# Performance work log

Measured on AMD Instinct MI355X. Metric: run time of the kernel, lower is better.

The kernel has to match this reference:

```python
import jax, jax.numpy as jnp
import numpy as np

FORGET_BIAS = 1.0

def _lstm_scan(x_seq, W, b, c0, h0):
    """x_seq: [T, B, D]; W: [D+H, 4H] (gate order i,j,f,o as in BasicLSTMCell)."""
    def step(carry, x_t):
        c, h = carry
        gates = jnp.dot(jnp.concatenate([x_t, h], axis=-1), W) + b  # [B, 4H]
        i, j, f, o = jnp.split(gates, 4, axis=-1)
        c_new = c * jax.nn.sigmoid(f + FORGET_BIAS) + jax.nn.sigmoid(i) * jnp.tanh(j)
        h_new = jnp.tanh(c_new) * jax.nn.sigmoid(o)
        return (c_new, h_new), h_new
    (c_T, h_T), hs = jax.lax.scan(step, (c0, h0), x_seq)
    return hs, (c_T, h_T)


def setup_inputs() -> dict:
    key = jax.random.key(0)
    ks = jax.random.split(key, 10)
    B, T_enc, D_in = 128, 64, 2048
    T_dec, D_w, H, V = 32, 300, 512, 32000
    s = lambda fan_in: 1.0 / np.sqrt(fan_in)
    return {
        "frames": jax.random.normal(ks[0], (B, T_enc, D_in), dtype=jnp.float32),
        "caption_ids": jax.random.randint(ks[1], (B, T_dec), 0, V, dtype=jnp.int32),
        "emb_table": jax.random.normal(ks[2], (V, D_w), dtype=jnp.float32) * 0.1,
        "W_enc": jax.random.normal(ks[3], (D_in + H, 4 * H), dtype=jnp.float32) * s(D_in + H),
        "b_enc": jnp.zeros((4 * H,), dtype=jnp.float32),
        "W_dec": jax.random.normal(ks[4], (D_w + H, 4 * H), dtype=jnp.float32) * s(D_w + H),
        "b_dec": jnp.zeros((4 * H,), dtype=jnp.float32),
        "W_out": jax.random.normal(ks[5], (H, D_w), dtype=jnp.float32) * s(H),
        "b_out": jnp.zeros((D_w,), dtype=jnp.float32),
    }


def reference(frames, caption_ids, emb_table, W_enc, b_enc, W_dec, b_dec, W_out, b_out):
    B, _, _ = frames.shape
    H = W_out.shape[0]
    c0 = jnp.zeros((B, H), dtype=frames.dtype)
    h0 = jnp.zeros((B, H), dtype=frames.dtype)

    # Encoder: dynamic_rnn over frames (dropout keep_prob=1 -> identity)
    _, enc_state = _lstm_scan(jnp.swapaxes(frames, 0, 1), W_enc, b_enc, c0, h0)

    # Decoder: teacher-forced over caption embeddings, starting from encoder state
    cap_emb = emb_table[caption_ids]                       # [B, T_dec, D_w]
    dec_hs, _ = _lstm_scan(jnp.swapaxes(cap_emb, 0, 1), W_dec, b_dec, *enc_state)  # [T_dec, B, H]

    # hidden_to_word dense per timestep
    word_vecs = jnp.einsum('tbh,hw->tbw', dec_hs, W_out) + b_out  # [T_dec, B, D_w]
    return jnp.swapaxes(word_vecs, 0, 1)                   # [B, T_dec, D_w]
```

## Files before the change

kernel.cpp:

```cpp
#include <hip/hip_runtime.h>
#include <stdint.h>

typedef unsigned short u16;
typedef __attribute__((ext_vector_type(4))) float f32x4;
typedef __attribute__((ext_vector_type(8))) short short8;
typedef __attribute__((ext_vector_type(4))) unsigned short u16x4;
typedef __attribute__((ext_vector_type(4))) int int4v;

__device__ __forceinline__ u16 f2b(float f) {
  uint32_t u = __float_as_uint(f);
  uint32_t r = (u + 0x7fffu + ((u >> 16) & 1u)) >> 16;
  return (u16)r;
}
__device__ __forceinline__ float b2f(u16 b) {
  return __uint_as_float(((uint32_t)b) << 16);
}
__device__ __forceinline__ float sigm(float x) { return 1.f / (1.f + __expf(-x)); }
__device__ __forceinline__ float tanh_fast(float x) {
  float e = __expf(2.f * x);
  return 1.f - 2.f / (e + 1.f);
}
__device__ __forceinline__ void gl2lds16(const void* g, void* l) {
  __builtin_amdgcn_global_load_lds((const __attribute__((address_space(1))) void*)g,
                                   (__attribute__((address_space(3))) void*)l, 16, 0, 0);
}

__global__ void cvt_bf16_kernel(const float* __restrict__ in, u16* __restrict__ out, int n4) {
  int i = blockIdx.x * 256 + threadIdx.x;
  if (i >= n4) return;
  float4 v = ((const float4*)in)[i];
  u16x4 o = { f2b(v.x), f2b(v.y), f2b(v.z), f2b(v.w) };
  *(u16x4*)(out + (size_t)i * 4) = o;
}

__global__ void transpose_kernel(const float* __restrict__ W, u16* __restrict__ WT,
                                 int ldin, int ldout, int xreal, int xpad) {
  __shared__ float tile[64][65];
  const int kb = blockIdx.x * 64;
  const int pb = blockIdx.y * 64;
  const int t = threadIdx.x;
  const int pc = t & 63;
  const int kr4 = t >> 6;
#pragma unroll
  for (int it = 0; it < 16; ++it) {
    int kl = kr4 + it * 4;
    int kc = kb + kl;
    int ko = kc < xpad ? kc : kc - (xpad - xreal);
    bool valid = (kc < xreal) || (kc >= xpad);
    tile[kl][pc] = valid ? W[(size_t)ko * ldin + pb + pc] : 0.f;
  }
  __syncthreads();
  const int pl = t >> 2;
  const int kq = t & 3;
#pragma unroll
  for (int half = 0; half < 2; ++half) {
    union { short8 v; u16 a[8]; } pk;
#pragma unroll
    for (int i = 0; i < 8; ++i) pk.a[i] = f2b(tile[kq * 16 + half * 8 + i][pl]);
    *(short8*)&WT[(size_t)(pb + pl) * ldout + kb + kq * 16 + half * 8] = pk.v;
  }
}

__global__ void woutT_kernel(const float* __restrict__ Wout, u16* __restrict__ WT) {
  int idx = blockIdx.x * 256 + threadIdx.x;
  if (idx >= 384 * 512) return;
  int n = idx >> 9, k = idx & 511;
  float v = (n < 300) ? Wout[(size_t)k * 300 + n] : 0.f;
  WT[idx] = f2b(v);
}

__global__ void embed_kernel(const int* __restrict__ ids, const float* __restrict__ emb,
                             u16* __restrict__ Adec) {
  int r = blockIdx.x;
  int t = r >> 7, b = r & 127;
  int id = ids[b * 32 + t];
  const float* src = emb + (size_t)id * 300;
  u16* dst = Adec + (size_t)r * 320;
  for (int d = threadIdx.x; d < 320; d += 64)
    dst[d] = f2b(d < 300 ? src[d] : 0.f);
}

template <int MODE>
__global__ __launch_bounds__(256)
void gemm_kernel(const u16* __restrict__ A, int lda,
                 const u16* __restrict__ BT, int ldb,
                 void* __restrict__ Cv, const float* __restrict__ bias, int K) {
  __shared__ u16 atile[128 * 32];
  __shared__ u16 btile[128 * 32];
  const int tid = threadIdx.x;
  const int wave = tid >> 6;
  const int lane = tid & 63;
  const int m0 = blockIdx.x * 128;
  const int n0 = blockIdx.y * 128;
  const int wm = wave & 1;
  const int wn = wave >> 1;
  const int colq = lane & 15;
  const int rquad = lane >> 4;

  f32x4 acc[4][4];
#pragma unroll
  for (int i = 0; i < 4; ++i)
#pragma unroll
    for (int j = 0; j < 4; ++j) { f32x4 z = {0.f, 0.f, 0.f, 0.f}; acc[i][j] = z; }

  for (int k0 = 0; k0 < K; k0 += 32) {
#pragma unroll
    for (int c = 0; c < 2; ++c) {
      const int ch = wave + c * 4;
      const int slot = ch * 64 + lane;
      const int m = slot >> 2;
      const int koff = (slot & 3) * 8;
      gl2lds16(A + (size_t)(m0 + m) * lda + k0 + koff, atile + ch * 512);
      gl2lds16(BT + (size_t)(n0 + m) * ldb + k0 + koff, btile + ch * 512);
    }
    __builtin_amdgcn_s_waitcnt(0);
    __syncthreads();
    short8 af[4], bf[4];
#pragma unroll
    for (int i = 0; i < 4; ++i)
      af[i] = *(const short8*)(atile + (wm * 64 + i * 16 + colq) * 32 + rquad * 8);
#pragma unroll
    for (int j = 0; j < 4; ++j)
      bf[j] = *(const short8*)(btile + (wn * 64 + j * 16 + colq) * 32 + rquad * 8);
#pragma unroll
    for (int i = 0; i < 4; ++i)
#pragma unroll
      for (int j = 0; j < 4; ++j)
        acc[i][j] = __builtin_amdgcn_mfma_f32_16x16x32_bf16(af[i], bf[j], acc[i][j], 0, 0, 0);
    __syncthreads();
  }

  const int gm_base = m0 + wm * 64;
  const int gn_base = n0 + wn * 64;
#pragma unroll
  for (int i = 0; i < 4; ++i) {
#pragma unroll
    for (int j = 0; j < 4; ++j) {
      const int gn = gn_base + j * 16 + colq;
      float bv;
      if (MODE == 2) bv = (gn < 300) ? bias[gn] : 0.f;
      else bv = bias[gn];
      const int rbase = gm_base + i * 16 + rquad * 4;
#pragma unroll
      for (int r = 0; r < 4; ++r) {
        const float v = acc[i][j][r] + bv;
        const int row = rbase + r;
        if (MODE == 0) {
          ((u16*)Cv)[(size_t)((row & 63) * 128 + (row >> 6)) * 2048 + gn] = f2b(v);
        } else if (MODE == 1) {
          ((u16*)Cv)[(size_t)row * 2048 + gn] = f2b(v);
        } else {
          if (gn < 300)
            ((float*)Cv)[(size_t)((row & 127) * 32 + (row >> 7)) * 300 + gn] = v;
        }
      }
    }
  }
}

__global__ __launch_bounds__(128)
void lstm_recurrent_kernel(const u16* __restrict__ pre_enc,
                           const u16* __restrict__ pre_dec,
                           const u16* __restrict__ WencT,
                           const u16* __restrict__ WdecT,
                           int* __restrict__ hbuf,
                           u16* __restrict__ dec_hs,
                           int* __restrict__ flags) {
  const int tid = threadIdx.x;
  const int lane = tid & 63;
  const int hb = tid >> 6;
  const int bg = blockIdx.x & 7;
  const int hg = blockIdx.x >> 3;
  const int colq = lane & 15;
  const int rquad = lane >> 4;

  __shared__ u16 wlds[128][520];
  __shared__ u16 stage[2][16][32];

  {
    for (int i = tid; i < 128 * 64; i += 128) {
      int lr = i >> 6, cc = i & 63;
      const u16* src = WencT + (size_t)((lr >> 5) * 512 + hg * 32 + (lr & 31)) * 2560 + 2048;
      *(short8*)&wlds[lr][cc * 8] = *(const short8*)(src + cc * 8);
    }
  }
  __syncthreads();

  float cst[4] = {0.f, 0.f, 0.f, 0.f};
  const int brow = bg * 16 + rquad * 4;
  const int pbase = hg * 32 + hb * 16 + colq;

  union HV { int4v i; short8 s; };

  for (int s = 0; s < 96; ++s) {
    const bool dec = (s >= 64);
    const u16* pre_t = dec ? (pre_dec + (size_t)(s - 64) * 262144)
                           : (pre_enc + (size_t)s * 262144);
    f32x4 acc[4];
#pragma unroll
    for (int l = 0; l < 4; ++l)
#pragma unroll
      for (int r = 0; r < 4; ++r)
        acc[l][r] = b2f(pre_t[(size_t)(brow + r) * 2048 + l * 512 + pbase]);

    if (s > 0) {
      const int* fp = flags + ((size_t)s * 8 + bg) * 16 + (lane & 15);
      while (__hip_atomic_load(fp, __ATOMIC_RELAXED, __HIP_MEMORY_SCOPE_AGENT) == 0) {}
      asm volatile("" ::: "memory");
    }

    HV hv[16];
    const int* hread = hbuf + (size_t)s * 32768 + bg * 4096 + colq * 16 + rquad * 4;
#pragma unroll
    for (int g = 0; g < 4; ++g) {
      const int* hp = hread + g * 1024;
#pragma unroll
      for (int q = 0; q < 4; ++q)
        asm volatile("global_load_dwordx4 %0, %1, off offset:%2 sc0 sc1"
                     : "=v"(hv[g * 4 + q].i) : "v"(hp), "i"(q * 1024) : "memory");
    }
    asm volatile("s_waitcnt vmcnt(0)" ::: "memory");
#pragma unroll
    for (int kt = 0; kt < 16; ++kt)
      asm volatile("" : "+v"(hv[kt].i));

#pragma unroll
    for (int kt = 0; kt < 16; ++kt) {
#pragma unroll
      for (int l = 0; l < 4; ++l) {
        short8 bf = *(const short8*)&wlds[l * 32 + hb * 16 + colq][kt * 32 + rquad * 8];
        acc[l] = __builtin_amdgcn_mfma_f32_16x16x32_bf16(hv[kt].s, bf, acc[l], 0, 0, 0);
      }
    }

    const int sb = s & 1;
#pragma unroll
    for (int r = 0; r < 4; ++r) {
      float iv = acc[0][r], jv = acc[1][r], fv = acc[2][r], ov = acc[3][r];
      float cn = cst[r] * sigm(fv + 1.f) + sigm(iv) * tanh_fast(jv);
      cst[r] = cn;
      float hvv = tanh_fast(cn) * sigm(ov);
      stage[sb][rquad * 4 + r][hb * 16 + colq] = f2b(hvv);
    }
    __syncthreads();

    if (tid < 64) {
      const int row = tid >> 2, q = tid & 3;
      union { short8 v; int4v i; } vv;
      vv.v = *(const short8*)&stage[sb][row][q * 8];
      int* dst = hbuf + (size_t)(s + 1) * 32768 + bg * 4096 + hg * 256 + row * 16 + q * 4;
      asm volatile("global_store_dwordx4 %0, %1, off sc0 sc1"
                   :: "v"(dst), "v"(vv.i) : "memory");
      if (dec)
        *(short8*)&dec_hs[(size_t)(s - 64) * 65536 + (size_t)(bg * 16 + row) * 512 +
                          hg * 32 + q * 8] = vv.v;
      asm volatile("s_waitcnt vmcnt(0)" ::: "memory");
      if (tid == 0) {
        int* fp = flags + ((size_t)(s + 1) * 8 + bg) * 16 + hg;
        int one = 1;
        asm volatile("global_store_dword %0, %1, off sc0 sc1"
                     :: "v"(fp), "v"(one) : "memory");
      }
    }

    if (s == 63) {
      for (int i = tid; i < 128 * 64; i += 128) {
        int lr = i >> 6, cc = i & 63;
        const u16* src = WdecT + (size_t)((lr >> 5) * 512 + hg * 32 + (lr & 31)) * 832 + 320;
        *(short8*)&wlds[lr][cc * 8] = *(const short8*)(src + cc * 8);
      }
      __syncthreads();
    }
  }
  asm volatile("s_waitcnt vmcnt(0)" ::: "memory");
}

extern "C" void kernel_launch(void* const* d_in, const int* in_sizes, int n_in,
                              void* d_out, int out_size, void* d_ws, size_t ws_size,
                              hipStream_t stream) {
  const float* frames = (const float*)d_in[0];
  const int* cap_ids  = (const int*)d_in[1];
  const float* emb    = (const float*)d_in[2];
  const float* W_enc  = (const float*)d_in[3];
  const float* b_enc  = (const float*)d_in[4];
  const float* W_dec  = (const float*)d_in[5];
  const float* b_dec  = (const float*)d_in[6];
  const float* W_out  = (const float*)d_in[7];
  const float* b_out  = (const float*)d_in[8];
  float* out = (float*)d_out;

  char* ws = (char*)d_ws;
  size_t off = 0;
  auto alloc = [&](size_t bytes) {
    void* p = ws + off;
    off += (bytes + 255) & ~(size_t)255;
    return p;
  };
  u16* A_enc   = (u16*)alloc(8192ull * 2048 * 2);
  u16* WencT   = (u16*)alloc(2048ull * 2560 * 2);
  u16* pre_enc = (u16*)alloc(64ull * 128 * 2048 * 2);
  u16* A_dec   = (u16*)alloc(4096ull * 320 * 2);
  u16* WdecT   = (u16*)alloc(2048ull * 832 * 2);
  u16* pre_dec = (u16*)alloc(32ull * 128 * 2048 * 2);
  u16* WoutT   = (u16*)alloc(384ull * 512 * 2);
  u16* dec_hs  = (u16*)alloc(32ull * 128 * 512 * 2);
  int* hbuf    = (int*)alloc(97ull * 32768 * 4);
  int* flags   = (int*)alloc(97ull * 8 * 16 * 4);

  hipMemsetAsync(hbuf, 0, 32768ull * 4, stream);
  hipMemsetAsync(flags, 0, 97ull * 8 * 16 * 4, stream);

  cvt_bf16_kernel<<<16384, 256, 0, stream>>>(frames, A_enc, 4194304);
  transpose_kernel<<<dim3(40, 32), 256, 0, stream>>>(W_enc, WencT, 2048, 2560, 2048, 2048);
  transpose_kernel<<<dim3(13, 32), 256, 0, stream>>>(W_dec, WdecT, 2048, 832, 300, 320);
  woutT_kernel<<<768, 256, 0, stream>>>(W_out, WoutT);
  embed_kernel<<<4096, 64, 0, stream>>>(cap_ids, emb, A_dec);

  gemm_kernel<0><<<dim3(64, 16), 256, 0, stream>>>(A_enc, 2048, WencT, 2560, pre_enc, b_enc, 2048);
  gemm_kernel<1><<<dim3(32, 16), 256, 0, stream>>>(A_dec, 320, WdecT, 832, pre_dec, b_dec, 320);

  lstm_recurrent_kernel<<<128, 128, 0, stream>>>(pre_enc, pre_dec, WencT, WdecT,
                                                 hbuf, dec_hs, flags);

  gemm_kernel<2><<<dim3(32, 3), 256, 0, stream>>>(dec_hs, 512, WoutT, 512, out, b_out, 512);
}
```

Measured before the change: 687.4 us.

## Fuse input-projection GEMMs and LSTM recurrence into one persistent kernel with per-timestep flags

Merges the encoder and decoder input-projection GEMMs with the recurrent LSTM kernel into a single launch. The first 128 blocks run the recurrence and spin on a per-timestep counter until the GEMM blocks for that timestep have written their pre-activations. The input conversion now writes frames in time-major order, so each GEMM tile of 128 rows maps to one timestep. It also double-buffers the GEMM LDS tiles using direct global-to-LDS loads. The aim is to overlap the serial recurrence with the large projection GEMM instead of running them back to back. The risk is a deadlock if the recurrent blocks are not resident, plus contention between the spinning blocks and the GEMM blocks.

```diff
diff --git a/kernel.cpp b/kernel.cpp
--- a/kernel.cpp
+++ b/kernel.cpp
@@ -29,8 +29,13 @@
   int i = blockIdx.x * 256 + threadIdx.x;
   if (i >= n4) return;
   float4 v = ((const float4*)in)[i];
+  int e = i * 4;
+  int b = e >> 17;
+  int t = (e >> 11) & 63;
+  int d = e & 2047;
+  size_t row = (size_t)t * 128 + b;
   u16x4 o = { f2b(v.x), f2b(v.y), f2b(v.z), f2b(v.w) };
-  *(u16x4*)(out + (size_t)i * 4) = o;
+  *(u16x4*)(out + row * 2048 + d) = o;
 }
 
 __global__ void transpose_kernel(const float* __restrict__ W, u16* __restrict__ WT,
@@ -80,11 +85,225 @@
     dst[d] = f2b(d < 300 ? src[d] : 0.f);
 }
 
-template <int MODE>
+struct SmemLstm { u16 wlds[128][520]; u16 stage[2][16][32]; };
+struct SmemGemm { u16 at[2][128 * 32]; u16 bt[2][128 * 32]; };
+union SmemU { SmemLstm l; SmemGemm g; };
+
 __global__ __launch_bounds__(256)
-void gemm_kernel(const u16* __restrict__ A, int lda,
-                 const u16* __restrict__ BT, int ldb,
-                 void* __restrict__ Cv, const float* __restrict__ bias, int K) {
+void mega_kernel(const u16* __restrict__ A_enc, const u16* __restrict__ WencT,
+                 u16* __restrict__ pre_enc, const float* __restrict__ b_enc,
+                 const u16* __restrict__ A_dec, const u16* __restrict__ WdecT,
+                 u16* __restrict__ pre_dec, const float* __restrict__ b_dec,
+                 int* __restrict__ hbuf, u16* __restrict__ dec_hs,
+                 int* __restrict__ flags, int* __restrict__ pf_enc,
+                 int* __restrict__ pf_dec) {
+  __shared__ SmemU sm;
+  const int bid = blockIdx.x;
+  const int tid = threadIdx.x;
+  const int lane = tid & 63;
+
+  if (bid < 128) {
+    const int hb = tid >> 6;
+    const int bg = bid & 7;
+    const int hg = bid >> 3;
+    const int colq = lane & 15;
+    const int rquad = lane >> 4;
+
+    for (int i = tid; i < 128 * 64; i += 256) {
+      int lr = i >> 6, cc = i & 63;
+      const u16* src = WencT + (size_t)((lr >> 5) * 512 + hg * 32 + (lr & 31)) * 2560 + 2048;
+      *(short8*)&sm.l.wlds[lr][cc * 8] = *(const short8*)(src + cc * 8);
+    }
+    __syncthreads();
+
+    float cst[4] = {0.f, 0.f, 0.f, 0.f};
+    const int brow = bg * 16 + rquad * 4;
+    const int pbase = hg * 32 + (hb & 1) * 16 + colq;
+    union HV { int4v i; short8 s; };
+
+    for (int s = 0; s < 96; ++s) {
+      const bool dec = (s >= 64);
+      const int sb = s & 1;
+      if (hb < 2) {
+        const u16* pre_t = dec ? (pre_dec + (size_t)(s - 64) * 262144)
+                               : (pre_enc + (size_t)s * 262144);
+        int* pf = dec ? (pf_dec + (s - 64)) : (pf_enc + s);
+        while (__hip_atomic_load(pf, __ATOMIC_RELAXED, __HIP_MEMORY_SCOPE_AGENT) != 16) {}
+        asm volatile("" ::: "memory");
+        int praw[4][4];
+        const u16* p0 = pre_t + (size_t)brow * 2048 + pbase;
+#pragma unroll
+        for (int l = 0; l < 4; ++l)
+#pragma unroll
+          for (int r = 0; r < 4; ++r)
+            asm volatile("global_load_ushort %0, %1, off sc0 sc1"
+                         : "=v"(praw[l][r]) : "v"(p0 + (size_t)r * 2048 + l * 512) : "memory");
+        if (s > 0) {
+          const int* fp = flags + ((size_t)s * 8 + bg) * 16 + (lane & 15);
+          while (__hip_atomic_load(fp, __ATOMIC_RELAXED, __HIP_MEMORY_SCOPE_AGENT) == 0) {}
+          asm volatile("" ::: "memory");
+        }
+        HV hv[16];
+        const int* hread = hbuf + (size_t)s * 32768 + bg * 4096 + colq * 16 + rquad * 4;
+#pragma unroll
+        for (int g = 0; g < 4; ++g) {
+          const int* hp = hread + g * 1024;
+#pragma unroll
+          for (int q = 0; q < 4; ++q)
+            asm volatile("global_load_dwordx4 %0, %1, off offset:%2 sc0 sc1"
+                         : "=v"(hv[g * 4 + q].i) : "v"(hp), "i"(q * 1024) : "memory");
+        }
+        asm volatile("s_waitcnt vmcnt(0)" ::: "memory");
+        __builtin_amdgcn_sched_barrier(0);
+#pragma unroll
+        for (int kt = 0; kt < 16; ++kt) asm volatile("" : "+v"(hv[kt].i));
+#pragma unroll
+        for (int l = 0; l < 4; ++l)
+#pragma unroll
+          for (int r = 0; r < 4; ++r) asm volatile("" : "+v"(praw[l][r]));
+        f32x4 acc[4];
+#pragma unroll
+        for (int l = 0; l < 4; ++l)
+#pragma unroll
+          for (int r = 0; r < 4; ++r) acc[l][r] = b2f((u16)praw[l][r]);
+#pragma unroll
+        for (int kt = 0; kt < 16; ++kt) {
+#pragma unroll
+          for (int l = 0; l < 4; ++l) {
+            short8 bf = *(const short8*)&sm.l.wlds[l * 32 + hb * 16 + colq][kt * 32 + rquad * 8];
+            acc[l] = __builtin_amdgcn_mfma_f32_16x16x32_bf16(hv[kt].s, bf, acc[l], 0, 0, 0);
+          }
+        }
+#pragma unroll
+        for (int r = 0; r < 4; ++r) {
+          float iv = acc[0][r], jv = acc[1][r], fv = acc[2][r], ov = acc[3][r];
+          float cn = cst[r] * sigm(fv + 1.f) + sigm(iv) * tanh_fast(jv);
+          cst[r] = cn;
+          float hvv = tanh_fast(cn) * sigm(ov);
+          sm.l.stage[sb][rquad * 4 + r][hb * 16 + colq] = f2b(hvv);
+        }
+      }
+      __syncthreads();
+      if (hb == 2) {
+        const int t2 = tid - 128;
+        const int row = t2 >> 2, q = t2 & 3;
+        union { short8 v; int4v i; } vv;
+        vv.v = *(const short8*)&sm.l.stage[sb][row][q * 8];
+        int* dst = hbuf + (size_t)(s + 1) * 32768 + bg * 4096 + hg * 256 + row * 16 + q * 4;
+        asm volatile("global_store_dwordx4 %0, %1, off sc0 sc1"
+                     :: "v"(dst), "v"(vv.i) : "memory");
+        if (dec)
+          *(short8*)&dec_hs[(size_t)(s - 64) * 65536 + (size_t)(bg * 16 + row) * 512 +
+                            hg * 32 + q * 8] = vv.v;
+        asm volatile("s_waitcnt vmcnt(0)" ::: "memory");
+        if (t2 == 0) {
+          int* fp = flags + ((size_t)(s + 1) * 8 + bg) * 16 + hg;
+          int one = 1;
+          asm volatile("global_store_dword %0, %1, off sc0 sc1"
+                       :: "v"(fp), "v"(one) : "memory");
+        }
+      }
+      if (s == 63) {
+        for (int i = tid; i < 128 * 64; i += 256) {
+          int lr = i >> 6, cc = i & 63;
+          const u16* src = WdecT + (size_t)((lr >> 5) * 512 + hg * 32 + (lr & 31)) * 832 + 320;
+          *(short8*)&sm.l.wlds[lr][cc * 8] = *(const short8*)(src + cc * 8);
+        }
+        __syncthreads();
+      }
+    }
+    asm volatile("s_waitcnt vmcnt(0)" ::: "memory");
+    return;
+  }
+
+  int idx = bid - 128;
+  const u16* A; const u16* BT; u16* C; const float* bias; int* flag;
+  int lda, ldb, K, m0, n0;
+  if (idx < 1024) {
+    int t = idx >> 4, nt = idx & 15;
+    A = A_enc; lda = 2048; BT = WencT; ldb = 2560; K = 2048;
+    C = pre_enc; bias = b_enc; flag = pf_enc + t;
+    m0 = t * 128; n0 = nt * 128;
+  } else {
+    idx -= 1024;
+    int t = idx >> 4, nt = idx & 15;
+    A = A_dec; lda = 320; BT = WdecT; ldb = 832; K = 320;
+    C = pre_dec; bias = b_dec; flag = pf_dec + t;
+    m0 = t * 128; n0 = nt * 128;
+  }
+  const int wave = tid >> 6;
+  const int wm = wave & 1, wn = wave >> 1;
+  const int colq = lane & 15, rquad = lane >> 4;
+
+  f32x4 acc[4][4];
+#pragma unroll
+  for (int i = 0; i < 4; ++i)
+#pragma unroll
+    for (int j = 0; j < 4; ++j) { f32x4 z = {0.f, 0.f, 0.f, 0.f}; acc[i][j] = z; }
+
+  auto stage_tile = [&](int buf, int k0) {
+#pragma unroll
+    for (int c = 0; c < 2; ++c) {
+      const int ch = wave + c * 4;
+      const int slot = ch * 64 + lane;
+      const int m = slot >> 2;
+      const int koff = (slot & 3) * 8;
+      gl2lds16(A + (size_t)(m0 + m) * lda + k0 + koff, sm.g.at[buf] + ch * 512);
+      gl2lds16(BT + (size_t)(n0 + m) * ldb + k0 + koff, sm.g.bt[buf] + ch * 512);
+    }
+  };
+
+  stage_tile(0, 0);
+  __builtin_amdgcn_s_waitcnt(0);
+  __syncthreads();
+  const int niter = K >> 5;
+  for (int it = 0; it < niter; ++it) {
+    const int cur = it & 1;
+    if (it + 1 < niter) stage_tile(cur ^ 1, (it + 1) << 5);
+    short8 af[4], bf[4];
+#pragma unroll
+    for (int i = 0; i < 4; ++i)
+      af[i] = *(const short8*)(sm.g.at[cur] + (wm * 64 + i * 16 + colq) * 32 + rquad * 8);
+#pragma unroll
+    for (int j = 0; j < 4; ++j)
+      bf[j] = *(const short8*)(sm.g.bt[cur] + (wn * 64 + j * 16 + colq) * 32 + rquad * 8);
+#pragma unroll
+    for (int i = 0; i < 4; ++i)
+#pragma unroll
+      for (int j = 0; j < 4; ++j)
+        acc[i][j] = __builtin_amdgcn_mfma_f32_16x16x32_bf16(af[i], bf[j], acc[i][j], 0, 0, 0);
+    __builtin_amdgcn_s_waitcnt(0);
+    __syncthreads();
+  }
+
+  const int gm_base = m0 + wm * 64;
+  const int gn_base = n0 + wn * 64;
+#pragma unroll
+  for (int i = 0; i < 4; ++i) {
+#pragma unroll
+    for (int j = 0; j < 4; ++j) {
+      const int gn = gn_base + j * 16 + colq;
+      const float bv = bias[gn];
+      const int rbase = gm_base + i * 16 + rquad * 4;
+#pragma unroll
+      for (int r = 0; r < 4; ++r) {
+        int hv16 = (int)f2b(acc[i][j][r] + bv);
+        const u16* addr = C + (size_t)(rbase + r) * 2048 + gn;
+        asm volatile("global_store_short %0, %1, off sc0 sc1"
+                     :: "v"(addr), "v"(hv16) : "memory");
+      }
+    }
+  }
+  asm volatile("s_waitcnt vmcnt(0)" ::: "memory");
+  __syncthreads();
+  if (tid == 0)
+    __hip_atomic_fetch_add(flag, 1, __ATOMIC_RELAXED, __HIP_MEMORY_SCOPE_AGENT);
+}
+
+__global__ __launch_bounds__(256)
+void out_gemm_kernel(const u16* __restrict__ A, const u16* __restrict__ BT,
+                     float* __restrict__ Cv, const float* __restrict__ bias) {
+  const int lda = 512, ldb = 512, K = 512;
   __shared__ u16 atile[128 * 32];
   __shared__ u16 btile[128 * 32];
   const int tid = threadIdx.x;
@@ -137,142 +356,17 @@
 #pragma unroll
     for (int j = 0; j < 4; ++j) {
       const int gn = gn_base + j * 16 + colq;
-      float bv;
-      if (MODE == 2) bv = (gn < 300) ? bias[gn] : 0.f;
-      else bv = bias[gn];
+      const float bv = (gn < 300) ? bias[gn] : 0.f;
       const int rbase = gm_base + i * 16 + rquad * 4;
 #pragma unroll
       for (int r = 0; r < 4; ++r) {
         const float v = acc[i][j][r] + bv;
         const int row = rbase + r;
-        if (MODE == 0) {
-          ((u16*)Cv)[(size_t)((row & 63) * 128 + (row >> 6)) * 2048 + gn] = f2b(v);
-        } else if (MODE == 1) {
-          ((u16*)Cv)[(size_t)row * 2048 + gn] = f2b(v);
-        } else {
-          if (gn < 300)
-            ((float*)Cv)[(size_t)((row & 127) * 32 + (row >> 7)) * 300 + gn] = v;
-        }
+        if (gn < 300)
+          Cv[(size_t)((row & 127) * 32 + (row >> 7)) * 300 + gn] = v;
       }
     }
   }
-}
-
-__global__ __launch_bounds__(128)
-void lstm_recurrent_kernel(const u16* __restrict__ pre_enc,
-                           const u16* __restrict__ pre_dec,
-                           const u16* __restrict__ WencT,
-                           const u16* __restrict__ WdecT,
-                           int* __restrict__ hbuf,
-                           u16* __restrict__ dec_hs,
-                           int* __restrict__ flags) {
-  const int tid = threadIdx.x;
-  const int lane = tid & 63;
-  const int hb = tid >> 6;
-  const int bg = blockIdx.x & 7;
-  const int hg = blockIdx.x >> 3;
-  const int colq = lane & 15;
-  const int rquad = lane >> 4;
-
-  __shared__ u16 wlds[128][520];
-  __shared__ u16 stage[2][16][32];
-
-  {
-    for (int i = tid; i < 128 * 64; i += 128) {
-      int lr = i >> 6, cc = i & 63;
-      const u16* src = WencT + (size_t)((lr >> 5) * 512 + hg * 32 + (lr & 31)) * 2560 + 2048;
-      *(short8*)&wlds[lr][cc * 8] = *(const short8*)(src + cc * 8);
-    }
-  }
-  __syncthreads();
-
-  float cst[4] = {0.f, 0.f, 0.f, 0.f};
-  const int brow = bg * 16 + rquad * 4;
-  const int pbase = hg * 32 + hb * 16 + colq;
-
-  union HV { int4v i; short8 s; };
-
-  for (int s = 0; s < 96; ++s) {
-    const bool dec = (s >= 64);
-    const u16* pre_t = dec ? (pre_dec + (size_t)(s - 64) * 262144)
-                           : (pre_enc + (size_t)s * 262144);
-    f32x4 acc[4];
-#pragma unroll
-    for (int l = 0; l < 4; ++l)
-#pragma unroll
-      for (int r = 0; r < 4; ++r)
-        acc[l][r] = b2f(pre_t[(size_t)(brow + r) * 2048 + l * 512 + pbase]);
-
-    if (s > 0) {
-      const int* fp = flags + ((size_t)s * 8 + bg) * 16 + (lane & 15);
-      while (__hip_atomic_load(fp, __ATOMIC_RELAXED, __HIP_MEMORY_SCOPE_AGENT) == 0) {}
-      asm volatile("" ::: "memory");
-    }
-
-    HV hv[16];
-    const int* hread = hbuf + (size_t)s * 32768 + bg * 4096 + colq * 16 + rquad * 4;
-#pragma unroll
-    for (int g = 0; g < 4; ++g) {
-      const int* hp = hread + g * 1024;
-#pragma unroll
-      for (int q = 0; q < 4; ++q)
-        asm volatile("global_load_dwordx4 %0, %1, off offset:%2 sc0 sc1"
-                     : "=v"(hv[g * 4 + q].i) : "v"(hp), "i"(q * 1024) : "memory");
-    }
-    asm volatile("s_waitcnt vmcnt(0)" ::: "memory");
-#pragma unroll
-    for (int kt = 0; kt < 16; ++kt)
-      asm volatile("" : "+v"(hv[kt].i));
-
-#pragma unroll
-    for (int kt = 0; kt < 16; ++kt) {
-#pragma unroll
-      for (int l = 0; l < 4; ++l) {
-        short8 bf = *(const short8*)&wlds[l * 32 + hb * 16 + colq][kt * 32 + rquad * 8];
-        acc[l] = __builtin_amdgcn_mfma_f32_16x16x32_bf16(hv[kt].s, bf, acc[l], 0, 0, 0);
-      }
-    }
-
-    const int sb = s & 1;
-#pragma unroll
-    for (int r = 0; r < 4; ++r) {
-      float iv = acc[0][r], jv = acc[1][r], fv = acc[2][r], ov = acc[3][r];
-      float cn = cst[r] * sigm(fv + 1.f) + sigm(iv) * tanh_fast(jv);
-      cst[r] = cn;
-      float hvv = tanh_fast(cn) * sigm(ov);
-      stage[sb][rquad * 4 + r][hb * 16 + colq] = f2b(hvv);
-    }
-    __syncthreads();
-
-    if (tid < 64) {
-      const int row = tid >> 2, q = tid & 3;
-      union { short8 v; int4v i; } vv;
-      vv.v = *(const short8*)&stage[sb][row][q * 8];
-      int* dst = hbuf + (size_t)(s + 1) * 32768 + bg * 4096 + hg * 256 + row * 16 + q * 4;
-      asm volatile("global_store_dwordx4 %0, %1, off sc0 sc1"
-                   :: "v"(dst), "v"(vv.i) : "memory");
-      if (dec)
-        *(short8*)&dec_hs[(size_t)(s - 64) * 65536 + (size_t)(bg * 16 + row) * 512 +
-                          hg * 32 + q * 8] = vv.v;
-      asm volatile("s_waitcnt vmcnt(0)" ::: "memory");
-      if (tid == 0) {
-        int* fp = flags + ((size_t)(s + 1) * 8 + bg) * 16 + hg;
-        int one = 1;
-        asm volatile("global_store_dword %0, %1, off sc0 sc1"
-                     :: "v"(fp), "v"(one) : "memory");
-      }
-    }
-
-    if (s == 63) {
-      for (int i = tid; i < 128 * 64; i += 128) {
-        int lr = i >> 6, cc = i & 63;
-        const u16* src = WdecT + (size_t)((lr >> 5) * 512 + hg * 32 + (lr & 31)) * 832 + 320;
-        *(short8*)&wlds[lr][cc * 8] = *(const short8*)(src + cc * 8);
-      }
-      __syncthreads();
-    }
-  }
-  asm volatile("s_waitcnt vmcnt(0)" ::: "memory");
 }
 
 extern "C" void kernel_launch(void* const* d_in, const int* in_sizes, int n_in,
@@ -306,9 +400,13 @@
   u16* dec_hs  = (u16*)alloc(32ull * 128 * 512 * 2);
   int* hbuf    = (int*)alloc(97ull * 32768 * 4);
   int* flags   = (int*)alloc(97ull * 8 * 16 * 4);
+  int* pf      = (int*)alloc(96ull * 4);
+  int* pf_enc  = pf;
+  int* pf_dec  = pf + 64;
 
   hipMemsetAsync(hbuf, 0, 32768ull * 4, stream);
   hipMemsetAsync(flags, 0, 97ull * 8 * 16 * 4, stream);
+  hipMemsetAsync(pf, 0, 96ull * 4, stream);
 
   cvt_bf16_kernel<<<16384, 256, 0, stream>>>(frames, A_enc, 4194304);
   transpose_kernel<<<dim3(40, 32), 256, 0, stream>>>(W_enc, WencT, 2048, 2560, 2048, 2048);
@@ -316,11 +414,9 @@
   woutT_kernel<<<768, 256, 0, stream>>>(W_out, WoutT);
   embed_kernel<<<4096, 64, 0, stream>>>(cap_ids, emb, A_dec);
 
-  gemm_kernel<0><<<dim3(64, 16), 256, 0, stream>>>(A_enc, 2048, WencT, 2560, pre_enc, b_enc, 2048);
-  gemm_kernel<1><<<dim3(32, 16), 256, 0, stream>>>(A_dec, 320, WdecT, 832, pre_dec, b_dec, 320);
-
-  lstm_recurrent_kernel<<<128, 128, 0, stream>>>(pre_enc, pre_dec, WencT, WdecT,
-                                                 hbuf, dec_hs, flags);
-
-  gemm_kernel<2><<<dim3(32, 3), 256, 0, stream>>>(dec_hs, 512, WoutT, 512, out, b_out, 512);
-}
+  mega_kernel<<<1664, 256, 0, stream>>>(A_enc, WencT, pre_enc, b_enc,
+                                        A_dec, WdecT, pre_dec, b_dec,
+                                        hbuf, dec_hs, flags, pf_enc, pf_dec);
+
+  out_gemm_kernel<<<dim3(32, 3), 256, 0, stream>>>(dec_hs, WoutT, out, b_out);
+}
```

Result: slower. 727.2 us (+5.8%).
